# Kernel optimization log

Measured on AMD Instinct MI355X. Metric: run time of the kernel, lower is better.

The kernel has to match this reference:

```python
import jax, jax.numpy as jnp
import numpy as np

S, B, H = 1024, 2, 1024
NH, NKV, HD = 16, 4, 64
E, TOPK, F = 8, 2, 2048
EPS = 1e-5


def _layer_norm(x, w, b):
    mu = jnp.mean(x, axis=-1, keepdims=True)
    var = jnp.mean(jnp.square(x - mu), axis=-1, keepdims=True)
    return (x - mu) * jax.lax.rsqrt(var + EPS) * w + b


def setup_inputs() -> dict:
    key = jax.random.key(0)
    ks = jax.random.split(key, 8)
    return {
        "hidden_states": jax.random.normal(ks[0], (S, B, H), jnp.float32),
        "ln1_weight": jnp.ones((H,), jnp.float32),
        "ln1_bias": jnp.zeros((H,), jnp.float32),
        "ln2_weight": jnp.ones((H,), jnp.float32),
        "ln2_bias": jnp.zeros((H,), jnp.float32),
        "qkv_weight": jax.random.normal(ks[1], ((NH + 2 * NKV) * HD, H), jnp.float32) * 0.02,
        "proj_weight": jax.random.normal(ks[2], (H, H), jnp.float32) * 0.02,
        "router_weight": jax.random.normal(ks[3], (E, H), jnp.float32) * 0.02,
        "moe_w1": jax.random.normal(ks[4], (E, H, F), jnp.float32) * 0.02,
        "moe_w2": jax.random.normal(ks[5], (E, F, H), jnp.float32) * 0.02,
    }


def reference(hidden_states, ln1_weight, ln1_bias, ln2_weight, ln2_bias,
              qkv_weight, proj_weight, router_weight, moe_w1, moe_w2):
    dtype = hidden_states.dtype
    # LN1 -> QKV projection
    ln1_out = _layer_norm(hidden_states, ln1_weight, ln1_bias)            # [S,B,H]
    qkv = jnp.einsum('sbh,oh->sbo', ln1_out, qkv_weight)                  # [S,B,(NH+2NKV)*HD]
    q = qkv[..., : NH * HD].reshape(S, B, NH, HD)
    k = qkv[..., NH * HD: (NH + NKV) * HD].reshape(S, B, NKV, HD)
    v = qkv[..., (NH + NKV) * HD:].reshape(S, B, NKV, HD)
    # GQA: expand kv heads (repeat_interleave along head dim)
    ratio = NH // NKV
    k = jnp.repeat(k, ratio, axis=2)                                      # [S,B,NH,HD]
    v = jnp.repeat(v, ratio, axis=2)
    # [S,B,h,d] -> [B,h,S,d]
    qb = jnp.transpose(q, (1, 2, 0, 3))
    kb = jnp.transpose(k, (1, 2, 0, 3))
    vb = jnp.transpose(v, (1, 2, 0, 3))
    scale = 1.0 / np.sqrt(HD)
    scores = jnp.einsum('bhqd,bhkd->bhqk', qb, kb) * scale                # [B,NH,S,S]
    causal = jnp.tril(jnp.ones((S, S), bool))
    scores = jnp.where(causal, scores, jnp.finfo(dtype).min)
    attn = jax.nn.softmax(scores, axis=-1)
    attn_out = jnp.einsum('bhqk,bhkd->bhqd', attn, vb)                    # [B,NH,S,HD]
    attn_out = jnp.transpose(attn_out, (2, 0, 1, 3)).reshape(S, B, H)     # [S,B,H]
    proj_out = jnp.einsum('sbh,oh->sbo', attn_out, proj_weight)
    hidden_after_attn = hidden_states + proj_out
    # LN2 -> MoE
    ln2_flat = _layer_norm(hidden_after_attn, ln2_weight, ln2_bias).reshape(-1, H)  # [T,H]
    logits = jnp.einsum('th,eh->te', ln2_flat, router_weight)             # [T,E]
    probs = jax.nn.softmax(logits, axis=-1)
    top_probs, top_idx = jax.lax.top_k(probs, TOPK)                       # [T,K]
    # combine gate: sum_k prob_k * onehot(expert_k)  -> [T,E]
    gate = jnp.sum(jax.nn.one_hot(top_idx, E, dtype=dtype) * top_probs[..., None], axis=1)
    # dense all-expert grouped GEMM equivalent of dispatch/FC1/act/FC2/combine
    h1 = jnp.einsum('th,ehf->tef', ln2_flat, moe_w1)                      # [T,E,F]
    a1 = jax.nn.gelu(h1)
    y = jnp.einsum('tef,efh->teh', a1, moe_w2)                            # [T,E,H]
    moe_out = jnp.einsum('te,teh->th', gate, y).reshape(S, B, H)
    return hidden_after_attn + moe_out
```

## Files before the change

kernel.cpp:

```cpp
#include <hip/hip_runtime.h>
#include <hip/hip_bf16.h>

typedef unsigned short u16;
typedef __attribute__((ext_vector_type(8))) short s16x8;
typedef __attribute__((ext_vector_type(4))) short s16x4;
typedef __attribute__((ext_vector_type(4))) float f32x4;

#define SEQ 1024
#define BATCH 2
#define HID 1024
#define NHEAD 16
#define NKVH 4
#define HDIM 64
#define NEXP 8
#define FFN 2048
#define TOK (SEQ*BATCH)
#define QKVO ((NHEAD + 2*NKVH)*HDIM)
#define NPART 80
#define PREC 2112

#define GL16(gp, lp) __builtin_amdgcn_global_load_lds( \
    (const __attribute__((address_space(1))) unsigned int*)(gp), \
    (__attribute__((address_space(3))) unsigned int*)(lp), 16, 0, 0)

__device__ __forceinline__ float b2f(u16 u) {
    unsigned int x = ((unsigned int)u) << 16;
    return __uint_as_float(x);
}
__device__ __forceinline__ u16 f2b(float f) {
    unsigned int x = __float_as_uint(f);
    x = (x + 0x7FFFu + ((x >> 16) & 1u)) >> 16;
    return (u16)x;
}
__device__ __forceinline__ void split2(float x, u16& hi, u16& lo) {
    hi = f2b(x);
    lo = f2b(x - b2f(hi));
}
__device__ __forceinline__ f32x4 mfma16(s16x8 a, s16x8 b, f32x4 c) {
    return __builtin_amdgcn_mfma_f32_16x16x32_bf16(a, b, c, 0, 0, 0);
}
__device__ __forceinline__ float gelu_t(float x) {
    float x3 = x * x * x;
    return 0.5f * x * (1.0f + tanhf(0.7978845608028654f * (x + 0.044715f * x3)));
}

template<int OUTMODE>
__global__ __launch_bounds__(256) void ln_k(const float* __restrict__ xin,
    const float* __restrict__ wgt, const float* __restrict__ bia,
    float* __restrict__ outf, u16* __restrict__ outh, u16* __restrict__ outl)
{
    __shared__ float red[8];
    const int t = blockIdx.x, tid = threadIdx.x;
    f32x4 u = *((const f32x4*)(xin + (size_t)t * HID) + tid);
    float s = u[0] + u[1] + u[2] + u[3];
    #pragma unroll
    for (int off = 32; off >= 1; off >>= 1) s += __shfl_xor(s, off);
    if ((tid & 63) == 0) red[tid >> 6] = s;
    __syncthreads();
    float mu = (red[0] + red[1] + red[2] + red[3]) * (1.0f / HID);
    float d0 = u[0]-mu, d1 = u[1]-mu, d2 = u[2]-mu, d3 = u[3]-mu;
    float ss = d0*d0 + d1*d1 + d2*d2 + d3*d3;
    #pragma unroll
    for (int off = 32; off >= 1; off >>= 1) ss += __shfl_xor(ss, off);
    if ((tid & 63) == 0) red[4 + (tid >> 6)] = ss;
    __syncthreads();
    float var = (red[4] + red[5] + red[6] + red[7]) * (1.0f / HID);
    float rs = 1.0f / sqrtf(var + 1e-5f);
    f32x4 wv = *((const f32x4*)wgt + tid);
    f32x4 bv = *((const f32x4*)bia + tid);
    f32x4 o;
    o[0] = d0*rs*wv[0] + bv[0];
    o[1] = d1*rs*wv[1] + bv[1];
    o[2] = d2*rs*wv[2] + bv[2];
    o[3] = d3*rs*wv[3] + bv[3];
    if (OUTMODE == 0 || OUTMODE >= 3)
        *((f32x4*)(outf + (size_t)t * HID) + tid) = o;
    if (OUTMODE == 2 || OUTMODE == 3) {
        s16x4 h, l;
        #pragma unroll
        for (int j = 0; j < 4; ++j) {
            u16 hb, lb; split2(o[j], hb, lb);
            h[j] = (short)hb; l[j] = (short)lb;
        }
        *((s16x4*)(outh + (size_t)t * HID) + tid) = h;
        *((s16x4*)(outl + (size_t)t * HID) + tid) = l;
    }
    if (OUTMODE == 4) {
        s16x4 h;
        #pragma unroll
        for (int j = 0; j < 4; ++j) h[j] = (short)f2b(o[j]);
        *((s16x4*)(outh + (size_t)t * HID) + tid) = h;
    }
}

__global__ __launch_bounds__(256) void split_cast_k(const float* __restrict__ in,
    u16* __restrict__ hi, u16* __restrict__ lo)
{
    int i = blockIdx.x * 256 + threadIdx.x;
    f32x4 v = ((const f32x4*)in)[i];
    s16x4 h, l;
    #pragma unroll
    for (int j = 0; j < 4; ++j) {
        u16 hb, lb; split2(v[j], hb, lb);
        h[j] = (short)hb; l[j] = (short)lb;
    }
    ((s16x4*)hi)[i] = h;
    ((s16x4*)lo)[i] = l;
}

__global__ __launch_bounds__(256) void trans_cast_k(const float* __restrict__ in,
    u16* __restrict__ out, int R, int C)
{
    __shared__ float tile[64][65];
    const int e = blockIdx.z;
    const float* src = in + (size_t)e * R * C;
    u16* dst = out + (size_t)e * C * R;
    const int r0 = blockIdx.y * 64, c0 = blockIdx.x * 64;
    const int tr = threadIdx.x >> 2, tc = (threadIdx.x & 3) * 16;
    #pragma unroll
    for (int j = 0; j < 4; ++j) {
        f32x4 v = *(const f32x4*)(src + (size_t)(r0 + tr) * C + c0 + tc + j * 4);
        *(f32x4*)&tile[tr][tc + j * 4] = v;
    }
    __syncthreads();
    s16x8 o0, o1;
    #pragma unroll
    for (int j = 0; j < 8; ++j) o0[j] = (short)f2b(tile[tc + j][tr]);
    #pragma unroll
    for (int j = 0; j < 8; ++j) o1[j] = (short)f2b(tile[tc + 8 + j][tr]);
    u16* dp = dst + (size_t)(c0 + tr) * R + r0 + tc;
    *(s16x8*)dp = o0;
    *(s16x8*)(dp + 8) = o1;
}

template<int AMODE, int TERMS, int EPI, int TILE, int KU>
__global__ __launch_bounds__(256, 2) void gemm_db(
    const u16* __restrict__ Ah, const u16* __restrict__ Al,
    const u16* __restrict__ Bh, const u16* __restrict__ Bl,
    void* __restrict__ Cv, const float* __restrict__ RES, float* __restrict__ C2,
    const int* __restrict__ glist, const int* __restrict__ offs,
    const int* __restrict__ cnts, const float* __restrict__ slot_p,
    int M, int N, int K, int lda, int ldb, int ldc, long long bStrideE)
{
    constexpr int BM = (TILE == 2) ? 64 : 128;
    constexpr int BN = (TILE == 0) ? 128 : 64;
    constexpr int MI = (TILE == 0) ? 4 : ((TILE == 1) ? 2 : 1);
    constexpr bool A2 = (BM == 128);
    constexpr bool B2 = (BN == 128);
    __shared__ u16 AHs[2][KU][BM][32];
    __shared__ u16 ALs[(TERMS >= 2) ? 2 : 1][(TERMS >= 2) ? KU : 1][(TERMS >= 2) ? BM : 1][32];
    __shared__ u16 BHs[2][KU][BN][32];
    __shared__ u16 BLs[(TERMS >= 3) ? 2 : 1][(TERMS >= 3) ? KU : 1][(TERMS >= 3) ? BN : 1][32];

    const int tid = threadIdx.x;
    const int m0 = blockIdx.y * BM;
    const int n0 = blockIdx.x * BN;
    int off = 0, cnt = M;
    if (AMODE != 0) {
        const int e = blockIdx.z;
        off = offs[e]; cnt = cnts[e];
        if (m0 >= cnt) return;
        long long be = (long long)e * bStrideE;
        Bh += be;
        if (TERMS >= 3) Bl += be;
    }
    const int lane = tid & 63, w = tid >> 6;
    const int wmB = (TILE == 0) ? ((w >> 1) * 64) : (w * (BM / 4));
    const int wnB = (TILE == 0) ? ((w & 1) * 64) : 0;
    const int l16 = lane & 15, grp = lane >> 4;
    const int srow = lane >> 2, schk = (lane & 3) * 8;
    const int lrA = w * (BM / 4);
    const int lrB = w * (BN / 4);

    long long ga0, ga1 = 0;
    {
        int am0 = m0 + lrA + srow;
        int am1 = am0 + 16;
        long long r0, r1;
        if (AMODE == 0) { r0 = am0; r1 = am1; }
        else if (AMODE == 1) {
            r0 = glist[off + ((am0 < cnt) ? am0 : 0)];
            r1 = A2 ? glist[off + ((am1 < cnt) ? am1 : 0)] : 0;
        } else {
            r0 = off + ((am0 < cnt) ? am0 : 0);
            r1 = A2 ? (off + ((am1 < cnt) ? am1 : 0)) : 0;
        }
        ga0 = r0 * lda + schk;
        if (A2) ga1 = r1 * lda + schk;
    }
    const long long gb0 = (long long)(n0 + lrB + srow) * ldb + schk;
    const long long gb1 = gb0 + 16LL * ldb;

    auto stage = [&](int bf, int k0) {
        #pragma unroll
        for (int u = 0; u < KU; ++u) {
            const int ko = k0 + u * 32;
            GL16(Ah + ga0 + ko, &AHs[bf][u][lrA][0]);
            if constexpr (A2) GL16(Ah + ga1 + ko, &AHs[bf][u][lrA + 16][0]);
            if constexpr (TERMS >= 2) {
                GL16(Al + ga0 + ko, &ALs[bf][u][lrA][0]);
                if constexpr (A2) GL16(Al + ga1 + ko, &ALs[bf][u][lrA + 16][0]);
            }
            GL16(Bh + gb0 + ko, &BHs[bf][u][lrB][0]);
            if constexpr (B2) GL16(Bh + gb1 + ko, &BHs[bf][u][lrB + 16][0]);
            if constexpr (TERMS >= 3) {
                GL16(Bl + gb0 + ko, &BLs[bf][u][lrB][0]);
                if constexpr (B2) GL16(Bl + gb1 + ko, &BLs[bf][u][lrB + 16][0]);
            }
        }
    };

    f32x4 acc[MI][4];
    #pragma unroll
    for (int i = 0; i < MI; ++i)
        #pragma unroll
        for (int j = 0; j < 4; ++j) acc[i][j] = f32x4{0.f, 0.f, 0.f, 0.f};

    const int nk = K / (32 * KU);
    int cur = 0;
    stage(0, 0);
    __syncthreads();
    for (int t = 0; t < nk; ++t) {
        if (t + 1 < nk) stage(cur ^ 1, (t + 1) * 32 * KU);
        #pragma unroll
        for (int u = 0; u < KU; ++u) {
            s16x8 ah[MI], al[MI], bh[4], bl[4];
            #pragma unroll
            for (int i = 0; i < MI; ++i)
                ah[i] = *(const s16x8*)&AHs[cur][u][wmB + i * 16 + l16][grp * 8];
            if constexpr (TERMS >= 2) {
                #pragma unroll
                for (int i = 0; i < MI; ++i)
                    al[i] = *(const s16x8*)&ALs[cur][u][wmB + i * 16 + l16][grp * 8];
            }
            #pragma unroll
            for (int j = 0; j < 4; ++j)
                bh[j] = *(const s16x8*)&BHs[cur][u][wnB + j * 16 + l16][grp * 8];
            if constexpr (TERMS >= 3) {
                #pragma unroll
                for (int j = 0; j < 4; ++j)
                    bl[j] = *(const s16x8*)&BLs[cur][u][wnB + j * 16 + l16][grp * 8];
            }
            #pragma unroll
            for (int i = 0; i < MI; ++i) {
                #pragma unroll
                for (int j = 0; j < 4; ++j) {
                    acc[i][j] = mfma16(ah[i], bh[j], acc[i][j]);
                    if constexpr (TERMS >= 3) acc[i][j] = mfma16(ah[i], bl[j], acc[i][j]);
                    if constexpr (TERMS >= 2) acc[i][j] = mfma16(al[i], bh[j], acc[i][j]);
                }
            }
        }
        __syncthreads();
        cur ^= 1;
    }
    #pragma unroll
    for (int i = 0; i < MI; ++i) {
        #pragma unroll
        for (int j = 0; j < 4; ++j) {
            int col = n0 + wnB + j * 16 + l16;
            #pragma unroll
            for (int r = 0; r < 4; ++r) {
                int mr = m0 + wmB + i * 16 + grp * 4 + r;
                if (AMODE != 0 && mr >= cnt) continue;
                long long crow = (AMODE == 0) ? mr : (off + mr);
                float val = acc[i][j][r];
                if (EPI == 0) {
                    ((float*)Cv)[crow * ldc + col] = val;
                } else if (EPI == 1) {
                    ((float*)Cv)[crow * ldc + col] = val + RES[crow * ldc + col];
                } else if (EPI == 2) {
                    ((u16*)Cv)[crow * ldc + col] = f2b(gelu_t(val));
                } else if (EPI == 5) {
                    ((u16*)Cv)[crow * ldc + col] = f2b(val);
                } else {
                    float v2 = val + RES[crow * ldc + col];
                    ((float*)Cv)[crow * ldc + col] = v2;
                    C2[crow * ldc + col] = v2;
                }
            }
        }
    }
}

__global__ __launch_bounds__(256) void kvprep(const float* __restrict__ qkvf,
    u16* __restrict__ kTh, u16* __restrict__ kTl,
    u16* __restrict__ vTh, u16* __restrict__ vTl)
{
    __shared__ float tile[64][68];
    const int st = blockIdx.x * 64;
    const int b = blockIdx.y & 1, kvh = blockIdx.y >> 1;
    const int tid = threadIdx.x;
    #pragma unroll
    for (int h = 0; h < 4; ++h) {
        int c = tid + h * 256;
        int srow = c >> 4, dseg = c & 15;
        f32x4 v = *(const f32x4*)(qkvf + (size_t)((st + srow) * BATCH + b) * QKVO
                                  + (NHEAD + NKVH) * HDIM + kvh * HDIM + dseg * 4);
        *(f32x4*)&tile[srow][dseg * 4] = v;
    }
    {
        int row = tid >> 2, qseg = tid & 3;
        const float* kr = qkvf + (size_t)((st + row) * BATCH + b) * QKVO
                          + NHEAD * HDIM + kvh * HDIM + qseg * 16;
        size_t ko = ((size_t)((b * NKVH + kvh) * SEQ + st + row)) * HDIM + qseg * 16;
        #pragma unroll
        for (int c = 0; c < 4; ++c) {
            f32x4 x = *(const f32x4*)(kr + c * 4);
            s16x4 vh, vl;
            #pragma unroll
            for (int j = 0; j < 4; ++j) {
                u16 hb, lb; split2(x[j], hb, lb);
                vh[j] = (short)hb; vl[j] = (short)lb;
            }
            *(s16x4*)(kTh + ko + c * 4) = vh;
            *(s16x4*)(kTl + ko + c * 4) = vl;
        }
    }
    __syncthreads();
    #pragma unroll
    for (int h = 0; h < 2; ++h) {
        int c = tid + h * 256;
        int drow = c >> 3, sseg = c & 7;
        s16x8 vh, vl;
        #pragma unroll
        for (int j = 0; j < 8; ++j) {
            u16 hb, lb; split2(tile[sseg * 8 + j][drow], hb, lb);
            vh[j] = (short)hb; vl[j] = (short)lb;
        }
        size_t oo = ((size_t)((b * NKVH + kvh) * HDIM + drow)) * SEQ + st + sseg * 8;
        *(s16x8*)(vTh + oo) = vh;
        *(s16x8*)(vTl + oo) = vl;
    }
}

__global__ __launch_bounds__(64, 3) void attn_part(
    const float* __restrict__ qkvf,
    const u16* __restrict__ kTh, const u16* __restrict__ kTl,
    const u16* __restrict__ vTh, const u16* __restrict__ vTl,
    float* __restrict__ part)
{
    __shared__ u16 plh[32][40];
    __shared__ u16 pll[32][40];
    const int p = blockIdx.x;
    int qt, c;
    if (p < 32)      { c = 0; qt = p; }
    else if (p < 56) { c = 1; qt = p - 24; }
    else if (p < 72) { c = 2; qt = p - 40; }
    else             { c = 3; qt = p - 48; }
    const int h = blockIdx.y, b = blockIdx.z;
    const int kvh = h >> 2;
    const int lane = threadIdx.x, l16 = lane & 15, grp = lane >> 4;

    s16x8 qh[2][2], ql[2][2];
    #pragma unroll
    for (int mt = 0; mt < 2; ++mt) {
        const float* qb = qkvf + (size_t)((qt * 32 + mt * 16 + l16) * BATCH + b) * QKVO
                          + h * HDIM + grp * 8;
        #pragma unroll
        for (int ks = 0; ks < 2; ++ks) {
            #pragma unroll
            for (int j = 0; j < 8; ++j) {
                u16 hb, lb; split2(qb[ks * 32 + j], hb, lb);
                qh[mt][ks][j] = (short)hb; ql[mt][ks][j] = (short)lb;
            }
        }
    }
    float mrow[2][4], lsum[2][4];
    f32x4 o[2][4];
    #pragma unroll
    for (int mt = 0; mt < 2; ++mt) {
        #pragma unroll
        for (int r = 0; r < 4; ++r) { mrow[mt][r] = -__builtin_inff(); lsum[mt][r] = 0.f; }
        #pragma unroll
        for (int db = 0; db < 4; ++db) o[mt][db] = f32x4{0.f, 0.f, 0.f, 0.f};
    }

    const size_t kvbase = (size_t)(b * NKVH + kvh) * SEQ;
    const int kv0 = c * 256;
    const int kv_hi = min(kv0 + 256, qt * 32 + 32);
    const int nt = (kv_hi - kv0 + 31) >> 5;
    for (int jb = 0; jb < nt; ++jb) {
        const int kvb = kv0 + jb * 32;
        f32x4 s[2][2];
        #pragma unroll
        for (int t2 = 0; t2 < 2; ++t2) {
            size_t kb = (kvbase + kvb + t2 * 16 + l16) * HDIM + grp * 8;
            f32x4 z0 = f32x4{0.f, 0.f, 0.f, 0.f};
            f32x4 z1 = f32x4{0.f, 0.f, 0.f, 0.f};
            #pragma unroll
            for (int ks = 0; ks < 2; ++ks) {
                s16x8 kh = *(const s16x8*)(kTh + kb + ks * 32);
                s16x8 kl = *(const s16x8*)(kTl + kb + ks * 32);
                z0 = mfma16(qh[0][ks], kh, z0);
                z0 = mfma16(qh[0][ks], kl, z0);
                z0 = mfma16(ql[0][ks], kh, z0);
                z1 = mfma16(qh[1][ks], kh, z1);
                z1 = mfma16(qh[1][ks], kl, z1);
                z1 = mfma16(ql[1][ks], kh, z1);
            }
            s[0][t2] = z0; s[1][t2] = z1;
        }
        #pragma unroll
        for (int mt = 0; mt < 2; ++mt) {
            #pragma unroll
            for (int r = 0; r < 4; ++r) {
                const int qrow = qt * 32 + mt * 16 + grp * 4 + r;
                float a0 = s[mt][0][r] * 0.125f; if (kvb + l16 > qrow) a0 = -__builtin_inff();
                float a1 = s[mt][1][r] * 0.125f; if (kvb + 16 + l16 > qrow) a1 = -__builtin_inff();
                float mx = fmaxf(a0, a1);
                #pragma unroll
                for (int t = 1; t < 16; t <<= 1) mx = fmaxf(mx, __shfl_xor(mx, t));
                float mn = fmaxf(mrow[mt][r], mx);
                float sc = __expf(mrow[mt][r] - mn);
                float p0 = __expf(a0 - mn), p1 = __expf(a1 - mn);
                float ps = p0 + p1;
                #pragma unroll
                for (int t = 1; t < 16; t <<= 1) ps += __shfl_xor(ps, t);
                lsum[mt][r] = lsum[mt][r] * sc + ps;
                mrow[mt][r] = mn;
                s[mt][0][r] = p0; s[mt][1][r] = p1;
                #pragma unroll
                for (int db = 0; db < 4; ++db) o[mt][db][r] *= sc;
            }
        }
        __syncthreads();
        #pragma unroll
        for (int mt = 0; mt < 2; ++mt) {
            #pragma unroll
            for (int t2 = 0; t2 < 2; ++t2) {
                #pragma unroll
                for (int r = 0; r < 4; ++r) {
                    u16 hb, lb; split2(s[mt][t2][r], hb, lb);
                    plh[mt * 16 + grp * 4 + r][t2 * 16 + l16] = hb;
                    pll[mt * 16 + grp * 4 + r][t2 * 16 + l16] = lb;
                }
            }
        }
        __syncthreads();
        s16x8 pah0 = *(const s16x8*)&plh[l16][grp * 8];
        s16x8 pal0 = *(const s16x8*)&pll[l16][grp * 8];
        s16x8 pah1 = *(const s16x8*)&plh[16 + l16][grp * 8];
        s16x8 pal1 = *(const s16x8*)&pll[16 + l16][grp * 8];
        #pragma unroll
        for (int db = 0; db < 4; ++db) {
            size_t vo = ((size_t)((b * NKVH + kvh) * HDIM + db * 16 + l16)) * SEQ + kvb + grp * 8;
            s16x8 vh = *(const s16x8*)(vTh + vo);
            s16x8 vl = *(const s16x8*)(vTl + vo);
            o[0][db] = mfma16(pah0, vh, o[0][db]);
            o[0][db] = mfma16(pah0, vl, o[0][db]);
            o[0][db] = mfma16(pal0, vh, o[0][db]);
            o[1][db] = mfma16(pah1, vh, o[1][db]);
            o[1][db] = mfma16(pah1, vl, o[1][db]);
            o[1][db] = mfma16(pal1, vh, o[1][db]);
        }
    }
    float* rec = part + (((size_t)(b * NHEAD + h) * NPART + p) * PREC);
    #pragma unroll
    for (int mt = 0; mt < 2; ++mt) {
        #pragma unroll
        for (int db = 0; db < 4; ++db) {
            #pragma unroll
            for (int r = 0; r < 4; ++r)
                rec[(mt * 16 + grp * 4 + r) * 64 + db * 16 + l16] = o[mt][db][r];
        }
    }
    if (l16 == 0) {
        #pragma unroll
        for (int mt = 0; mt < 2; ++mt) {
            #pragma unroll
            for (int r = 0; r < 4; ++r) {
                rec[2048 + mt * 16 + grp * 4 + r] = mrow[mt][r];
                rec[2080 + mt * 16 + grp * 4 + r] = lsum[mt][r];
            }
        }
    }
}

__global__ __launch_bounds__(256) void attn_comb(const float* __restrict__ part,
    u16* __restrict__ attn_h, u16* __restrict__ attn_l)
{
    const int qt16 = blockIdx.x, h = blockIdx.y, b = blockIdx.z;
    const int qt32 = qt16 >> 1;
    const int lrow = (qt16 & 1) * 16 + (threadIdx.x >> 4);
    const int nch = (qt32 >> 3) + 1;
    const int c4 = (threadIdx.x & 15) * 4;
    const size_t base = (size_t)(b * NHEAD + h) * NPART;
    const int pbase[4] = {0, 24, 40, 48};
    float mv[4], lv[4];
    float M = -__builtin_inff();
    #pragma unroll
    for (int c = 0; c < 4; ++c) {
        if (c < nch) {
            const float* rec = part + (base + pbase[c] + qt32) * PREC;
            mv[c] = rec[2048 + lrow];
            lv[c] = rec[2080 + lrow];
            M = fmaxf(M, mv[c]);
        }
    }
    float L = 0.f;
    f32x4 acc = f32x4{0.f, 0.f, 0.f, 0.f};
    #pragma unroll
    for (int c = 0; c < 4; ++c) {
        if (c < nch) {
            const float* rec = part + (base + pbase[c] + qt32) * PREC;
            float wgt = __expf(mv[c] - M);
            L += lv[c] * wgt;
            f32x4 ov = *(const f32x4*)(rec + lrow * 64 + c4);
            acc[0] += ov[0] * wgt; acc[1] += ov[1] * wgt;
            acc[2] += ov[2] * wgt; acc[3] += ov[3] * wgt;
        }
    }
    float inv = 1.f / L;
    const int qrow = qt32 * 32 + lrow;
    size_t oo = (size_t)(qrow * BATCH + b) * HID + h * HDIM + c4;
    #pragma unroll
    for (int j = 0; j < 4; ++j) {
        u16 hb, lb; split2(acc[j] * inv, hb, lb);
        attn_h[oo + j] = hb;
        attn_l[oo + j] = lb;
    }
}

__global__ __launch_bounds__(64) void router_k(const float* __restrict__ ln2,
    const float* __restrict__ rw, int* __restrict__ e01, float* __restrict__ p01,
    int* __restrict__ cnt)
{
    const int t = blockIdx.x, lane = threadIdx.x;
    const float* xr = ln2 + (size_t)t * HID + lane * 16;
    float x[16];
    #pragma unroll
    for (int c = 0; c < 4; ++c) {
        f32x4 u = *(const f32x4*)(xr + c * 4);
        #pragma unroll
        for (int j = 0; j < 4; ++j) x[c * 4 + j] = u[j];
    }
    float lg[8];
    #pragma unroll
    for (int e = 0; e < 8; ++e) {
        const float* wr = rw + (size_t)e * HID + lane * 16;
        float a = 0.f;
        #pragma unroll
        for (int c = 0; c < 4; ++c) {
            f32x4 wv = *(const f32x4*)(wr + c * 4);
            #pragma unroll
            for (int j = 0; j < 4; ++j) a += x[c * 4 + j] * wv[j];
        }
        #pragma unroll
        for (int off = 32; off >= 1; off >>= 1) a += __shfl_xor(a, off);
        lg[e] = a;
    }
    float mx = lg[0];
    #pragma unroll
    for (int e = 1; e < 8; ++e) mx = fmaxf(mx, lg[e]);
    float pe[8], ssum = 0.f;
    #pragma unroll
    for (int e = 0; e < 8; ++e) { pe[e] = expf(lg[e] - mx); ssum += pe[e]; }
    float inv = 1.f / ssum;
    int e0 = 0; float b0 = -1.f;
    #pragma unroll
    for (int e = 0; e < 8; ++e) { float p = pe[e] * inv; if (p > b0) { b0 = p; e0 = e; } }
    int e1 = -1; float b1 = -1.f;
    #pragma unroll
    for (int e = 0; e < 8; ++e) {
        if (e == e0) continue;
        float p = pe[e] * inv; if (p > b1) { b1 = p; e1 = e; }
    }
    if (lane == 0) {
        e01[2 * t] = e0; e01[2 * t + 1] = e1;
        p01[2 * t] = b0; p01[2 * t + 1] = b1;
        atomicAdd(&cnt[e0], 1); atomicAdd(&cnt[e1], 1);
    }
}

__global__ void init_k(int* cnt) {
    int i = threadIdx.x;
    if (i < 8) cnt[i] = 0;
}
__global__ void scan_k(const int* cnt, int* offs) {
    if (threadIdx.x == 0 && blockIdx.x == 0) {
        int a = 0;
        for (int e = 0; e < 8; ++e) { offs[e] = a; a += cnt[e]; }
    }
}
__global__ __launch_bounds__(64) void scatter_det(const int* __restrict__ e01,
    const float* __restrict__ p01, const int* __restrict__ offs,
    int* __restrict__ tok_of, float* __restrict__ slot_p, int* __restrict__ slot_of)
{
    const int e = blockIdx.x;
    const int lane = threadIdx.x;
    int base = offs[e];
    for (int c = 0; c < TOK; c += 64) {
        int t = c + lane;
        int kk = -1;
        if (e01[2 * t] == e) kk = 0;
        else if (e01[2 * t + 1] == e) kk = 1;
        int f = (kk >= 0) ? 1 : 0;
        int sc = f;
        #pragma unroll
        for (int o = 1; o < 64; o <<= 1) {
            int nn = __shfl_up(sc, o);
            if (lane >= o) sc += nn;
        }
        if (kk >= 0) {
            int slot = base + sc - 1;
            tok_of[slot] = t;
            slot_p[slot] = p01[2 * t + kk];
            slot_of[2 * t + kk] = slot;
        }
        base += __shfl(sc, 63);
    }
}

__global__ __launch_bounds__(256) void moe_comb(const u16* __restrict__ yb,
    const int* __restrict__ slot_of, const float* __restrict__ p01,
    float* __restrict__ out)
{
    const int t = blockIdx.x;
    const int c4 = threadIdx.x * 4;
    const int s0 = slot_of[2 * t], s1 = slot_of[2 * t + 1];
    const float p0 = p01[2 * t], p1 = p01[2 * t + 1];
    s16x4 y0 = *(const s16x4*)(yb + (size_t)s0 * HID + c4);
    s16x4 y1 = *(const s16x4*)(yb + (size_t)s1 * HID + c4);
    f32x4 o = *(f32x4*)(out + (size_t)t * HID + c4);
    #pragma unroll
    for (int j = 0; j < 4; ++j)
        o[j] += p0 * b2f((u16)y0[j]) + p1 * b2f((u16)y1[j]);
    *(f32x4*)(out + (size_t)t * HID + c4) = o;
}

__global__ void sentinel_k(float* out) {
    out[blockIdx.x * 256 + threadIdx.x] = 12345.0f;
}

extern "C" void kernel_launch(void* const* d_in, const int* in_sizes, int n_in,
                              void* d_out, int out_size, void* d_ws, size_t ws_size,
                              hipStream_t stream)
{
    (void)in_sizes; (void)n_in; (void)out_size;
    const float* hs    = (const float*)d_in[0];
    const float* ln1w  = (const float*)d_in[1];
    const float* ln1b  = (const float*)d_in[2];
    const float* ln2w  = (const float*)d_in[3];
    const float* ln2b  = (const float*)d_in[4];
    const float* qkvw  = (const float*)d_in[5];
    const float* projw = (const float*)d_in[6];
    const float* rw    = (const float*)d_in[7];
    const float* w1    = (const float*)d_in[8];
    const float* w2    = (const float*)d_in[9];
    float* out = (float*)d_out;
    char* ws = (char*)d_ws;

    size_t o = 0;
    auto alloc = [&](size_t bytes) -> void* {
        void* p = ws + o; o += (bytes + 255) & ~(size_t)255; return p;
    };
    u16*   w1t    = (u16*)alloc((size_t)NEXP * FFN * HID * 2);
    u16*   w2t    = (u16*)alloc((size_t)NEXP * HID * FFN * 2);
    u16*   qkvwh  = (u16*)alloc((size_t)QKVO * HID * 2);
    u16*   qkvwl  = (u16*)alloc((size_t)QKVO * HID * 2);
    u16*   projwh = (u16*)alloc((size_t)HID * HID * 2);
    u16*   projwl = (u16*)alloc((size_t)HID * HID * 2);
    u16*   ln1h   = (u16*)alloc((size_t)TOK * HID * 2);
    u16*   ln1l   = (u16*)alloc((size_t)TOK * HID * 2);
    float* qkvf   = (float*)alloc((size_t)TOK * QKVO * 4);
    u16*   kTh    = (u16*)alloc((size_t)BATCH * NKVH * SEQ * HDIM * 2);
    u16*   kTl    = (u16*)alloc((size_t)BATCH * NKVH * SEQ * HDIM * 2);
    u16*   vTh    = (u16*)alloc((size_t)BATCH * NKVH * HDIM * SEQ * 2);
    u16*   vTl    = (u16*)alloc((size_t)BATCH * NKVH * HDIM * SEQ * 2);
    float* haf    = (float*)alloc((size_t)TOK * HID * 4);
    u16*   ln2h   = (u16*)alloc((size_t)TOK * HID * 2);
    u16*   a1b    = (u16*)alloc((size_t)TOK * 2 * FFN * 2);
    int*   e01    = (int*)alloc(TOK * 2 * 4);
    float* p01    = (float*)alloc(TOK * 2 * 4);
    int*   cnt    = (int*)alloc(256);
    int*   offs   = (int*)alloc(256);
    int*   tok_of = (int*)alloc(TOK * 2 * 4);
    float* slot_p = (float*)alloc(TOK * 2 * 4);
    int*   slot_of = (int*)alloc(TOK * 2 * 4);
    size_t need = o;

    if (ws_size < need) {
        sentinel_k<<<TOK * HID / 256, 256, 0, stream>>>(out);
        return;
    }

    u16* attnh = ln1h;
    u16* attnl = ln1l;
    float* ln2f = qkvf;
    u16*  yb = (u16*)qkvf;
    float* part = (float*)w1t;

    split_cast_k<<<QKVO * HID / 4 / 256, 256, 0, stream>>>(qkvw, qkvwh, qkvwl);
    split_cast_k<<<HID * HID / 4 / 256, 256, 0, stream>>>(projw, projwh, projwl);
    ln_k<2><<<TOK, 256, 0, stream>>>(hs, ln1w, ln1b, nullptr, ln1h, ln1l);
    gemm_db<0, 3, 0, 2, 1><<<dim3(QKVO / 64, TOK / 64, 1), 256, 0, stream>>>(
        ln1h, ln1l, qkvwh, qkvwl, qkvf, nullptr, nullptr, nullptr, nullptr, nullptr, nullptr,
        TOK, QKVO, HID, HID, HID, QKVO, 0);
    kvprep<<<dim3(SEQ / 64, BATCH * NKVH), 256, 0, stream>>>(qkvf, kTh, kTl, vTh, vTl);
    attn_part<<<dim3(NPART, NHEAD, BATCH), 64, 0, stream>>>(
        qkvf, kTh, kTl, vTh, vTl, part);
    attn_comb<<<dim3(SEQ / 16, NHEAD, BATCH), 256, 0, stream>>>(part, attnh, attnl);
    gemm_db<0, 3, 4, 2, 1><<<dim3(HID / 64, TOK / 64, 1), 256, 0, stream>>>(
        attnh, attnl, projwh, projwl, haf, hs, out, nullptr, nullptr, nullptr, nullptr,
        TOK, HID, HID, HID, HID, HID, 0);
    ln_k<4><<<TOK, 256, 0, stream>>>(haf, ln2w, ln2b, ln2f, ln2h, nullptr);
    trans_cast_k<<<dim3(FFN / 64, HID / 64, NEXP), 256, 0, stream>>>(w1, w1t, HID, FFN);
    trans_cast_k<<<dim3(HID / 64, FFN / 64, NEXP), 256, 0, stream>>>(w2, w2t, FFN, HID);
    init_k<<<1, 64, 0, stream>>>(cnt);
    router_k<<<TOK, 64, 0, stream>>>(ln2f, rw, e01, p01, cnt);
    scan_k<<<1, 1, 0, stream>>>(cnt, offs);
    scatter_det<<<NEXP, 64, 0, stream>>>(e01, p01, offs, tok_of, slot_p, slot_of);
    gemm_db<1, 1, 2, 1, 2><<<dim3(FFN / 64, TOK / 128, NEXP), 256, 0, stream>>>(
        ln2h, nullptr, w1t, nullptr, a1b, nullptr, nullptr, tok_of, offs, cnt, nullptr,
        0, FFN, HID, HID, HID, FFN, (long long)FFN * HID);
    gemm_db<2, 1, 5, 1, 2><<<dim3(HID / 64, TOK / 128, NEXP), 256, 0, stream>>>(
        a1b, nullptr, w2t, nullptr, yb, nullptr, nullptr, tok_of, offs, cnt, slot_p,
        0, HID, FFN, FFN, FFN, HID, (long long)HID * FFN);
    moe_comb<<<TOK, 256, 0, stream>>>(yb, slot_of, p01, out);
}
```

Before: 350.6 us.

## Fold expert counting into scatter kernel, prefetch V tiles, vectorize Q loads

Drops the init and scan kernels and the per-token atomics from the router. Each scatter block now recounts expert assignments with a wave reduction to derive its own count and offset, removing two launches and their serialization. In the attention partial kernel, V tiles are loaded at the top of each KV iteration so the loads overlap the QK MFMAs and softmax, and Q is read with float4 vector loads. The cost is redundant counting work in every scatter block and more registers held live in the attention loop.

```diff
diff --git a/kernel.cpp b/kernel.cpp
--- a/kernel.cpp
+++ b/kernel.cpp
@@ -359,10 +359,15 @@
                           + h * HDIM + grp * 8;
         #pragma unroll
         for (int ks = 0; ks < 2; ++ks) {
-            #pragma unroll
-            for (int j = 0; j < 8; ++j) {
-                u16 hb, lb; split2(qb[ks * 32 + j], hb, lb);
+            f32x4 x0 = *(const f32x4*)(qb + ks * 32);
+            f32x4 x1 = *(const f32x4*)(qb + ks * 32 + 4);
+            #pragma unroll
+            for (int j = 0; j < 4; ++j) {
+                u16 hb, lb;
+                split2(x0[j], hb, lb);
                 qh[mt][ks][j] = (short)hb; ql[mt][ks][j] = (short)lb;
+                split2(x1[j], hb, lb);
+                qh[mt][ks][4 + j] = (short)hb; ql[mt][ks][4 + j] = (short)lb;
             }
         }
     }
@@ -382,6 +387,13 @@
     const int nt = (kv_hi - kv0 + 31) >> 5;
     for (int jb = 0; jb < nt; ++jb) {
         const int kvb = kv0 + jb * 32;
+        s16x8 vhv[4], vlv[4];
+        #pragma unroll
+        for (int db = 0; db < 4; ++db) {
+            size_t vo = ((size_t)((b * NKVH + kvh) * HDIM + db * 16 + l16)) * SEQ + kvb + grp * 8;
+            vhv[db] = *(const s16x8*)(vTh + vo);
+            vlv[db] = *(const s16x8*)(vTl + vo);
+        }
         f32x4 s[2][2];
         #pragma unroll
         for (int t2 = 0; t2 < 2; ++t2) {
@@ -444,15 +456,12 @@
         s16x8 pal1 = *(const s16x8*)&pll[16 + l16][grp * 8];
         #pragma unroll
         for (int db = 0; db < 4; ++db) {
-            size_t vo = ((size_t)((b * NKVH + kvh) * HDIM + db * 16 + l16)) * SEQ + kvb + grp * 8;
-            s16x8 vh = *(const s16x8*)(vTh + vo);
-            s16x8 vl = *(const s16x8*)(vTl + vo);
-            o[0][db] = mfma16(pah0, vh, o[0][db]);
-            o[0][db] = mfma16(pah0, vl, o[0][db]);
-            o[0][db] = mfma16(pal0, vh, o[0][db]);
-            o[1][db] = mfma16(pah1, vh, o[1][db]);
-            o[1][db] = mfma16(pah1, vl, o[1][db]);
-            o[1][db] = mfma16(pal1, vh, o[1][db]);
+            o[0][db] = mfma16(pah0, vhv[db], o[0][db]);
+            o[0][db] = mfma16(pah0, vlv[db], o[0][db]);
+            o[0][db] = mfma16(pal0, vhv[db], o[0][db]);
+            o[1][db] = mfma16(pah1, vhv[db], o[1][db]);
+            o[1][db] = mfma16(pah1, vlv[db], o[1][db]);
+            o[1][db] = mfma16(pal1, vhv[db], o[1][db]);
         }
     }
     float* rec = part + (((size_t)(b * NHEAD + h) * NPART + p) * PREC);
@@ -523,8 +532,7 @@
 }
 
 __global__ __launch_bounds__(64) void router_k(const float* __restrict__ ln2,
-    const float* __restrict__ rw, int* __restrict__ e01, float* __restrict__ p01,
-    int* __restrict__ cnt)
+    const float* __restrict__ rw, int* __restrict__ e01, float* __restrict__ p01)
 {
     const int t = blockIdx.x, lane = threadIdx.x;
     const float* xr = ln2 + (size_t)t * HID + lane * 16;
@@ -569,27 +577,32 @@
     if (lane == 0) {
         e01[2 * t] = e0; e01[2 * t + 1] = e1;
         p01[2 * t] = b0; p01[2 * t + 1] = b1;
-        atomicAdd(&cnt[e0], 1); atomicAdd(&cnt[e1], 1);
-    }
-}
-
-__global__ void init_k(int* cnt) {
-    int i = threadIdx.x;
-    if (i < 8) cnt[i] = 0;
-}
-__global__ void scan_k(const int* cnt, int* offs) {
-    if (threadIdx.x == 0 && blockIdx.x == 0) {
-        int a = 0;
-        for (int e = 0; e < 8; ++e) { offs[e] = a; a += cnt[e]; }
-    }
-}
+    }
+}
+
 __global__ __launch_bounds__(64) void scatter_det(const int* __restrict__ e01,
-    const float* __restrict__ p01, const int* __restrict__ offs,
+    const float* __restrict__ p01, int* __restrict__ cnt, int* __restrict__ offs,
     int* __restrict__ tok_of, float* __restrict__ slot_p, int* __restrict__ slot_of)
 {
     const int e = blockIdx.x;
     const int lane = threadIdx.x;
-    int base = offs[e];
+    int myc[8] = {0, 0, 0, 0, 0, 0, 0, 0};
+    for (int i = lane; i < 2 * TOK; i += 64) {
+        int ei = e01[i];
+        #pragma unroll
+        for (int ee = 0; ee < 8; ++ee) myc[ee] += (ei == ee) ? 1 : 0;
+    }
+    #pragma unroll
+    for (int ee = 0; ee < 8; ++ee) {
+        int v = myc[ee];
+        #pragma unroll
+        for (int off = 32; off >= 1; off >>= 1) v += __shfl_xor(v, off);
+        myc[ee] = v;
+    }
+    int base = 0;
+    #pragma unroll
+    for (int ee = 0; ee < 8; ++ee) if (ee < e) base += myc[ee];
+    if (lane == 0) { cnt[e] = myc[e]; offs[e] = base; }
     for (int c = 0; c < TOK; c += 64) {
         int t = c + lane;
         int kk = -1;
@@ -707,10 +720,8 @@
     ln_k<4><<<TOK, 256, 0, stream>>>(haf, ln2w, ln2b, ln2f, ln2h, nullptr);
     trans_cast_k<<<dim3(FFN / 64, HID / 64, NEXP), 256, 0, stream>>>(w1, w1t, HID, FFN);
     trans_cast_k<<<dim3(HID / 64, FFN / 64, NEXP), 256, 0, stream>>>(w2, w2t, FFN, HID);
-    init_k<<<1, 64, 0, stream>>>(cnt);
-    router_k<<<TOK, 64, 0, stream>>>(ln2f, rw, e01, p01, cnt);
-    scan_k<<<1, 1, 0, stream>>>(cnt, offs);
-    scatter_det<<<NEXP, 64, 0, stream>>>(e01, p01, offs, tok_of, slot_p, slot_of);
+    router_k<<<TOK, 64, 0, stream>>>(ln2f, rw, e01, p01);
+    scatter_det<<<NEXP, 64, 0, stream>>>(e01, p01, cnt, offs, tok_of, slot_p, slot_of);
     gemm_db<1, 1, 2, 1, 2><<<dim3(FFN / 64, TOK / 128, NEXP), 256, 0, stream>>>(
         ln2h, nullptr, w1t, nullptr, a1b, nullptr, nullptr, tok_of, offs, cnt, nullptr,
         0, FFN, HID, HID, HID, FFN, (long long)FFN * HID);
```

After: 326.2 us. 1.07x faster.
